# Kernel optimization log

Hardware: AMD Instinct MI355X
Metric: run time of the kernel (lower is better)

## Reference

```python
import jax, jax.numpy as jnp
import numpy as np

B, D, G, L = 8, 128, 2048, 24
GF = G // 2 + 1  # rfft bins
EPS = 1e-5


def setup_inputs() -> dict:
    key = jax.random.key(0)
    ks = jax.random.split(key, 6)
    x = jax.random.normal(ks[0], (B, D, G), dtype=jnp.float32)
    Phi_f = jax.random.normal(ks[1], (L, GF), dtype=jnp.float32) * 0.1
    Theta = jax.random.normal(ks[2], (L, D, D), dtype=jnp.float32) * (1.0 / np.sqrt(D))
    ln_gamma = jnp.ones((D,), dtype=jnp.float32)
    ln_beta = jnp.zeros((D,), dtype=jnp.float32)
    fc1_w = jax.random.normal(ks[3], (2 * D, D), dtype=jnp.float32) * (1.0 / np.sqrt(D))
    fc1_b = jnp.zeros((2 * D,), dtype=jnp.float32)
    fc2_w = jax.random.normal(ks[4], (D, 2 * D), dtype=jnp.float32) * (1.0 / np.sqrt(2 * D))
    fc2_b = jnp.zeros((D,), dtype=jnp.float32)
    return {
        'x': x, 'Phi_f': Phi_f, 'Theta': Theta,
        'ln_gamma': ln_gamma, 'ln_beta': ln_beta,
        'fc1_w': fc1_w, 'fc1_b': fc1_b, 'fc2_w': fc2_w, 'fc2_b': fc2_b,
    }


def reference(x, Phi_f, Theta, ln_gamma, ln_beta, fc1_w, fc1_b, fc2_w, fc2_b):
    # x: (B, D, G). LayerNorm over the lifting (channel) dim D.
    mean = jnp.mean(x, axis=1, keepdims=True)
    var = jnp.var(x, axis=1, keepdims=True)
    z = (x - mean) * jax.lax.rsqrt(var + EPS)
    z = z * ln_gamma[None, :, None] + ln_beta[None, :, None]

    # Spectral convolution with each Hilbert filter.
    Xf = jnp.fft.rfft(z, axis=-1)                       # (B, D, GF) complex
    Uf = Xf[:, :, None, :] * jnp.conj(Phi_f)[None, None]  # (B, D, L, GF)
    U = jnp.fft.irfft(Uf, n=G, axis=-1)                 # (B, D, L, G)

    # Per-filter channel mixing then reduction over filters:
    # einsum('bdln,lhd->bhln') followed by sum over l, fused:
    S = jnp.einsum('bdlg,lhd->bhg', U, Theta)           # (B, D, G)

    # Pointwise MLP (Conv1d kernel_size=1 == channel matmul).
    H = jnp.einsum('hd,bdg->bhg', fc1_w, S) + fc1_b[None, :, None]
    H = jax.nn.gelu(H, approximate=False)
    out = jnp.einsum('dh,bhg->bdg', fc2_w, H) + fc2_b[None, :, None]
    return x + out
```

## Files before the change

### kernel.cpp

```cpp
#include <hip/hip_runtime.h>
#include <math.h>


#define B_   8
#define D_   128
#define G_   2048
#define L_   24
#define GF_  1025
#define BD_  1024
#define DD_  16384
#define GQ_  512
#define CF4_ 514
#define MF4_ 576
#define NF4_ 4096

#define PA_CV0 256
#define PA_TT0 322
#define PA_WF0 578
#define PA_WI0 1154
#define PA_END 1666

#define G1_NB  576
#define G1_END 4800

typedef __attribute__((ext_vector_type(8))) short  short8v;
typedef __attribute__((ext_vector_type(4))) float  float4v;

union FU { float f; unsigned int u; };
union V8 { short8v v; ushort u[8]; };
union V4 { uint2 p; ushort u[4]; };

static __device__ __forceinline__ float bf2f(ushort h) {
    FU v; v.u = ((unsigned int)h) << 16; return v.f;
}
static __device__ __forceinline__ ushort f2bf(float f) {
    FU v; v.f = f;
    unsigned int r = v.u + 0x7fffu + ((v.u >> 16) & 1u);
    return (ushort)(r >> 16);
}
static __device__ __forceinline__ void async16(const void* g, void* l) {
    __builtin_amdgcn_global_load_lds(
        (const __attribute__((address_space(1))) void*)g,
        (__attribute__((address_space(3))) void*)l, 16, 0, 0);
}
static __device__ __forceinline__ int is_f32(const unsigned int* graw) {
    return graw[0] == 0x3F800000u;
}

__global__ __launch_bounds__(256) void k_pre(
        const void* __restrict__ x_raw,  const void* __restrict__ th_raw,
        const unsigned int* __restrict__ graw, const void* __restrict__ be_raw,
        const void* __restrict__ w1_raw, const void* __restrict__ b1_raw,
        const void* __restrict__ w2_raw, const void* __restrict__ b2_raw,
        ushort* __restrict__ z,  ushort* __restrict__ wf,
        ushort* __restrict__ wi, ushort* __restrict__ thT,
        ushort* __restrict__ w1c, ushort* __restrict__ b1c,
        ushort* __restrict__ w2c, ushort* __restrict__ b2c) {
    __shared__ ushort T[L_][72];
    __shared__ float red[2][256];
    __shared__ float mi[2][64];
    int bid = blockIdx.x, tid = threadIdx.x;

    if (bid < PA_CV0) {
        int fl = is_f32(graw);
        int b  = bid >> 5;
        int g0 = (bid & 31) * 64;
        int gi = tid & 63, dq = tid >> 6;
        int g  = g0 + gi;
        int d0 = dq * 32;
        float vals[32];
        float s = 0.f, ss = 0.f;
        if (fl) {
            const float* xp = (const float*)x_raw + (size_t)(b * D_ + d0) * G_ + g;
            #pragma unroll 8
            for (int d = 0; d < 32; ++d) {
                float v = xp[(size_t)d * G_];
                vals[d] = v; s += v; ss += v * v;
            }
        } else {
            const ushort* xp = (const ushort*)x_raw + (size_t)(b * D_ + d0) * G_ + g;
            #pragma unroll 8
            for (int d = 0; d < 32; ++d) {
                float v = bf2f(xp[(size_t)d * G_]);
                vals[d] = v; s += v; ss += v * v;
            }
        }
        red[0][tid] = s; red[1][tid] = ss;
        __syncthreads();
        if (tid < 64) {
            float S  = red[0][tid] + red[0][tid + 64] + red[0][tid + 128] +
                       red[0][tid + 192];
            float SS = red[1][tid] + red[1][tid + 64] + red[1][tid + 128] +
                       red[1][tid + 192];
            float mean = S * (1.f / D_);
            float var  = SS * (1.f / D_) - mean * mean;
            mi[0][tid] = mean;
            mi[1][tid] = rsqrtf(var + 1e-5f);
        }
        __syncthreads();
        float mean = mi[0][gi], inv = mi[1][gi];
        ushort* zp = z + (size_t)(g & 3) * (BD_ * GQ_) +
                     (size_t)(b * D_ + d0) * GQ_ + (g >> 2);
        if (fl) {
            const float* gp = (const float*)graw + d0;
            const float* bp = (const float*)be_raw + d0;
            #pragma unroll 8
            for (int d = 0; d < 32; ++d) {
                float o = (vals[d] - mean) * inv * gp[d] + bp[d];
                zp[(size_t)d * GQ_] = f2bf(o);
            }
        } else {
            const ushort* gp = (const ushort*)graw + d0;
            const ushort* bp = (const ushort*)be_raw + d0;
            #pragma unroll 8
            for (int d = 0; d < 32; ++d) {
                float o = (vals[d] - mean) * inv * bf2f(gp[d]) + bf2f(bp[d]);
                zp[(size_t)d * GQ_] = f2bf(o);
            }
        }
    } else if (bid < PA_TT0) {
        int fl = is_f32(graw);
        int lb = bid - PA_CV0;
        const void* src; ushort* dst; int n, rel;
        if (lb < 32)       { src = w1_raw; dst = w1c; n = 32768; rel = lb; }
        else if (lb == 32) { src = b1_raw; dst = b1c; n = 256;   rel = 0; }
        else if (lb < 65)  { src = w2_raw; dst = w2c; n = 32768; rel = lb - 33; }
        else               { src = b2_raw; dst = b2c; n = 128;   rel = 0; }
        int i0 = rel * 1024 + tid * 4;
        if (fl) {
            const float* s = (const float*)src;
            #pragma unroll
            for (int j = 0; j < 4; ++j) {
                int k = i0 + j;
                if (k < n) dst[k] = f2bf(s[k]);
            }
        } else {
            const ushort* s = (const ushort*)src;
            #pragma unroll
            for (int j = 0; j < 4; ++j) {
                int k = i0 + j;
                if (k < n) dst[k] = s[k];
            }
        }
    } else if (bid < PA_WF0) {
        int fl = is_f32(graw);
        int hd0 = (bid - PA_TT0) * 64;
        if (tid < 192) {
            int l = tid >> 3, c8 = tid & 7;
            V8 o;
            if (fl) {
                const float* tp = (const float*)th_raw + (size_t)l * DD_ +
                                  hd0 + c8 * 8;
                float4v a0 = *(const float4v*)tp;
                float4v a1 = *(const float4v*)(tp + 4);
                #pragma unroll
                for (int j = 0; j < 4; ++j) {
                    o.u[j] = f2bf(a0[j]); o.u[4 + j] = f2bf(a1[j]);
                }
            } else {
                o.v = *(const short8v*)((const ushort*)th_raw +
                                        (size_t)l * DD_ + hd0 + c8 * 8);
            }
            *(short8v*)&T[l][c8 * 8] = o.v;
        }
        __syncthreads();
        int hdl = tid & 63, part = tid >> 6;
        V8 o;
        #pragma unroll
        for (int j = 0; j < 8; ++j) {
            int l = part * 8 + j;
            o.u[j] = (l < L_) ? T[l][hdl] : (ushort)0;
        }
        *(short8v*)(thT + (size_t)(hd0 + hdl) * 32 + part * 8) = o.v;
    } else if (bid < PA_WI0) {
        int c = bid - PA_WF0;
        if (tid < 128) {
            int g0 = tid * 4;
            V4 v;
            if (c >= CF4_) {
                #pragma unroll
                for (int j = 0; j < 4; ++j) v.u[j] = 0;
            } else {
                int f = c >> 1, im = c & 1;
                #pragma unroll
                for (int j = 0; j < 4; ++j) {
                    int g = g0 + j;
                    int r = (f * g) & (GQ_ - 1);
                    float th = (float)r * 1.2271846303085130e-2f;
                    v.u[j] = f2bf(im ? -__sinf(th) : __cosf(th));
                }
            }
            *(uint2*)(wf + (size_t)c * GQ_ + g0) = v.p;
        }
    } else {
        int g = bid - PA_WI0;
        for (int ch = tid; ch < MF4_ / 8; ch += 256) {
            int c0 = ch * 8;
            V8 v;
            #pragma unroll
            for (int j = 0; j < 8; ++j) {
                int c = c0 + j;
                if (c >= CF4_) { v.u[j] = 0; continue; }
                int f = c >> 1, im = c & 1;
                float a = (f == 0 || f == GQ_ / 2) ? 4.8828125e-4f
                                                   : 9.765625e-4f;
                int r = (f * g) & (GQ_ - 1);
                float th = (float)r * 1.2271846303085130e-2f;
                v.u[j] = f2bf(im ? -a * __sinf(th) : a * __cosf(th));
            }
            *(short8v*)(wi + (size_t)g * MF4_ + c0) = v.v;
        }
    }
}

__global__ __launch_bounds__(256, 4) void k_g1(
        const ushort* __restrict__ wf, const ushort* __restrict__ z,
        ushort* __restrict__ zft,
        const void* __restrict__ phi_raw, const unsigned int* __restrict__ graw,
        const ushort* __restrict__ thT, ushort* __restrict__ M) {
    __shared__ ushort As[2][64 * 64];
    __shared__ ushort Bs[2][64 * 64];
    __shared__ ushort Aph[16][40];
    int bid = blockIdx.x, tid = threadIdx.x;
    int w = tid >> 6, lane = tid & 63;
    int lr = lane & 15, q = lane >> 4;

    if (bid < G1_NB) {
        int m0 = (bid >> 6) * 64;
        int n0 = (bid & 63) * 64;
        int wm = (w & 1) * 32, wn = (w >> 1) * 32;
        int rl = lane >> 3, c8 = (lane & 7) ^ rl;
        int t0 = w * 2, t1 = w * 2 + 1;
        const ushort* gA0 = wf + (size_t)(m0 + t0 * 8 + rl) * GQ_ + c8 * 8;
        const ushort* gA1 = wf + (size_t)(m0 + t1 * 8 + rl) * GQ_ + c8 * 8;
        const ushort* gB0 = z  + (size_t)(n0 + t0 * 8 + rl) * GQ_ + c8 * 8;
        const ushort* gB1 = z  + (size_t)(n0 + t1 * 8 + rl) * GQ_ + c8 * 8;

        float4v acc00 = {0.f,0.f,0.f,0.f}, acc01 = {0.f,0.f,0.f,0.f};
        float4v acc10 = {0.f,0.f,0.f,0.f}, acc11 = {0.f,0.f,0.f,0.f};

        async16(gA0, &As[0][t0 * 512]);
        async16(gA1, &As[0][t1 * 512]);
        async16(gB0, &Bs[0][t0 * 512]);
        async16(gB1, &Bs[0][t1 * 512]);
        __syncthreads();

        int buf = 0;
        for (int k0 = 0; k0 < GQ_; k0 += 64) {
            if (k0 + 64 < GQ_) {
                int nb = buf ^ 1;
                async16(gA0 + k0 + 64, &As[nb][t0 * 512]);
                async16(gA1 + k0 + 64, &As[nb][t1 * 512]);
                async16(gB0 + k0 + 64, &Bs[nb][t0 * 512]);
                async16(gB1 + k0 + 64, &Bs[nb][t1 * 512]);
            }
            const ushort* Ab = &As[buf][0];
            const ushort* Bb = &Bs[buf][0];
            #pragma unroll
            for (int s = 0; s < 2; ++s) {
                int cs = s * 4 + q;
                int ra0 = wm + lr, ra1 = wm + 16 + lr;
                int rb0 = wn + lr, rb1 = wn + 16 + lr;
                short8v a0 = *(const short8v*)(Ab + ra0 * 64 + ((cs ^ (ra0 & 7)) << 3));
                short8v a1 = *(const short8v*)(Ab + ra1 * 64 + ((cs ^ (ra1 & 7)) << 3));
                short8v b0 = *(const short8v*)(Bb + rb0 * 64 + ((cs ^ (rb0 & 7)) << 3));
                short8v b1 = *(const short8v*)(Bb + rb1 * 64 + ((cs ^ (rb1 & 7)) << 3));
                acc00 = __builtin_amdgcn_mfma_f32_16x16x32_bf16(a0, b0, acc00, 0, 0, 0);
                acc01 = __builtin_amdgcn_mfma_f32_16x16x32_bf16(a0, b1, acc01, 0, 0, 0);
                acc10 = __builtin_amdgcn_mfma_f32_16x16x32_bf16(a1, b0, acc10, 0, 0, 0);
                acc11 = __builtin_amdgcn_mfma_f32_16x16x32_bf16(a1, b1, acc11, 0, 0, 0);
            }
            __syncthreads();
            buf ^= 1;
        }

        float4v accs[2][2] = { { acc00, acc01 }, { acc10, acc11 } };
        #pragma unroll
        for (int i = 0; i < 2; ++i)
            #pragma unroll
            for (int j = 0; j < 2; ++j) {
                int col = n0 + wn + j * 16 + lr;
                int row = m0 + wm + i * 16 + q * 4;
                #pragma unroll
                for (int r = 0; r < 4; ++r)
                    zft[(size_t)(row + r) * NF4_ + col] = f2bf(accs[i][j][r]);
            }
    } else {
        int bb  = bid - G1_NB;
        int f0  = (bb >> 6) * 16;
        int hd0 = (bb & 63) * 256;
        int isf = is_f32(graw);
        #pragma unroll
        for (int rep = 0; rep < 2; ++rep) {
            int idx = rep * 256 + tid;
            int fl = idx >> 5, l = idx & 31;
            int f = f0 + fl;
            ushort v = 0;
            if (l < L_ && f < GF_)
                v = isf ? f2bf(((const float*)phi_raw)[(size_t)l * GF_ + f])
                        : ((const ushort*)phi_raw)[(size_t)l * GF_ + f];
            Aph[fl][l] = v;
        }
        __syncthreads();
        short8v a = *(const short8v*)&Aph[lr][q * 8];
        #pragma unroll
        for (int t = 0; t < 4; ++t) {
            int n = hd0 + (w * 4 + t) * 16 + lr;
            short8v b = *(const short8v*)(thT + (size_t)n * 32 + q * 8);
            float4v c = {0.f, 0.f, 0.f, 0.f};
            c = __builtin_amdgcn_mfma_f32_16x16x32_bf16(a, b, c, 0, 0, 0);
            #pragma unroll
            for (int r = 0; r < 4; ++r) {
                int f = f0 + q * 4 + r;
                if (f < GF_) M[(size_t)f * DD_ + n] = f2bf(c[r]);
            }
        }
    }
}

__global__ __launch_bounds__(256, 2) void k_mix3(const ushort* __restrict__ zft,
                                                 const ushort* __restrict__ M,
                                                 ushort* __restrict__ sft) {
    int bx  = blockIdx.x;
    int fp  = bx >> 1;
    int hh  = bx & 1;
    int tid = threadIdx.x;
    int w = tid >> 6, lane = tid & 63;
    int lr = lane & 15, q = lane >> 4;
    int cc = lr >> 3, bb = lr & 7;
    int ntg = hh * 4 + w;

    float a1 = (float)fp * 3.0679615757712823e-3f;
    float C1 = cosf(a1),        S1 = sinf(a1);
    float C2 = cosf(2.f * a1),  S2 = sinf(2.f * a1);
    float C3 = cosf(3.f * a1),  S3 = sinf(3.f * a1);

    float P01 = cc ? -S1 :  C1,  Q01 = cc ?  C1 :  S1;
    float P02 = cc ? -S2 :  C2,  Q02 = cc ?  C2 :  S2;
    float P03 = cc ? -S3 :  C3,  Q03 = cc ?  C3 :  S3;
    float P11 = cc ? -C1 :  S1,  Q11 = cc ? -S1 : -C1;
    float P12 = cc ? -S2 : -C2,  Q12 = cc ?  C2 : -S2;
    float P13 = cc ?  C3 : -S3,  Q13 = cc ?  S3 :  C3;
    float P21 = cc ? -C1 : -S1,  Q21 = cc ? -S1 :  C1;
    float P22 = cc ?  S2 : -C2,  Q22 = cc ? -C2 : -S2;
    float P23 = cc ?  C3 :  S3,  Q23 = cc ?  S3 : -C3;
    float P31 = cc ? -S1 : -C1,  Q31 = cc ?  C1 : -S1;
    float P32 = cc ?  S2 :  C2,  Q32 = cc ? -C2 :  S2;
    float P33 = cc ? -S3 : -C3,  Q33 = cc ?  C3 : -S3;

    const ushort* r0 = zft + (size_t)(2 * fp) * NF4_;
    const ushort* r1 = r0 + NF4_;
    int colb = bb * 128 + q * 8;

    short8v aZ[4][4];
    #pragma unroll
    for (int s = 0; s < 4; ++s) {
        int col = colb + s * 32;
        V8 R0, I0, R1, I1, R2, I2, R3, I3;
        R0.v = *(const short8v*)(r0 + col);
        I0.v = *(const short8v*)(r1 + col);
        R1.v = *(const short8v*)(r0 + 1024 + col);
        I1.v = *(const short8v*)(r1 + 1024 + col);
        R2.v = *(const short8v*)(r0 + 2048 + col);
        I2.v = *(const short8v*)(r1 + 2048 + col);
        R3.v = *(const short8v*)(r0 + 3072 + col);
        I3.v = *(const short8v*)(r1 + 3072 + col);
        V8 t0, t1, t2, t3;
        #pragma unroll
        for (int e = 0; e < 8; ++e) {
            float x0 = bf2f(R0.u[e]), y0 = bf2f(I0.u[e]);
            float x1 = bf2f(R1.u[e]), y1 = bf2f(I1.u[e]);
            float x2 = bf2f(R2.u[e]), y2 = bf2f(I2.u[e]);
            float x3 = bf2f(R3.u[e]), y3 = bf2f(I3.u[e]);
            float e0p = cc ?  y0 : x0;
            float e0m = cc ? -y0 : x0;
            float z0 = e0p, z1 = e0m, z2 = e0p, z3 = e0m;
            z0 = fmaf(P01, x1, z0); z0 = fmaf(Q01, y1, z0);
            z0 = fmaf(P02, x2, z0); z0 = fmaf(Q02, y2, z0);
            z0 = fmaf(P03, x3, z0); z0 = fmaf(Q03, y3, z0);
            z1 = fmaf(P11, x1, z1); z1 = fmaf(Q11, y1, z1);
            z1 = fmaf(P12, x2, z1); z1 = fmaf(Q12, y2, z1);
            z1 = fmaf(P13, x3, z1); z1 = fmaf(Q13, y3, z1);
            z2 = fmaf(P21, x1, z2); z2 = fmaf(Q21, y1, z2);
            z2 = fmaf(P22, x2, z2); z2 = fmaf(Q22, y2, z2);
            z2 = fmaf(P23, x3, z2); z2 = fmaf(Q23, y3, z2);
            z3 = fmaf(P31, x1, z3); z3 = fmaf(Q31, y1, z3);
            z3 = fmaf(P32, x2, z3); z3 = fmaf(Q32, y2, z3);
            z3 = fmaf(P33, x3, z3); z3 = fmaf(Q33, y3, z3);
            t0.u[e] = f2bf(z0); t1.u[e] = f2bf(z1);
            t2.u[e] = f2bf(z2); t3.u[e] = f2bf(z3);
        }
        aZ[0][s] = t0.v; aZ[1][s] = t1.v; aZ[2][s] = t2.v; aZ[3][s] = t3.v;
    }

    int fk0 = fp, fk1 = 512 - fp, fk2 = 512 + fp, fk3 = 1024 - fp;
    const ushort* Mp[4] = { M + (size_t)fk0 * DD_, M + (size_t)fk1 * DD_,
                            M + (size_t)fk2 * DD_, M + (size_t)fk3 * DD_ };
    float4v acc[4];
    #pragma unroll
    for (int k = 0; k < 4; ++k) {
        float4v c = {0.f, 0.f, 0.f, 0.f};
        #pragma unroll
        for (int s = 0; s < 4; ++s) {
            short8v bfr = *(const short8v*)(Mp[k] + (size_t)(ntg * 16 + lr) * D_ +
                                            s * 32 + q * 8);
            c = __builtin_amdgcn_mfma_f32_16x16x32_bf16(aZ[k][s], bfr, c, 0, 0, 0);
        }
        acc[k] = c;
    }

    #pragma unroll
    for (int e = 0; e < 4; ++e) {
        int p   = q * 4 + e;
        int c2i = p >> 3, cb = p & 7;
        float sg = c2i ? -1.f : 1.f;
        float u0 = acc[0][e], u1 = acc[1][e], u2 = acc[2][e], u3 = acc[3][e];
        float p1 = __shfl_xor(u1, 32);
        float p2 = __shfl_xor(u2, 32);
        float U0 = u0 + u2 + sg * (u1 + u3);
        float U1 = u0 - sg * p2 - sg * u3 - p1;
        float U2 = u0 - u2 + sg * (u3 - u1);
        float U3 = u0 + sg * p2 - sg * u3 + p1;
        float U1p = __shfl_xor(U1, 32);
        float U2p = __shfl_xor(U2, 32);
        float U3p = __shfl_xor(U3, 32);
        float T1 = fmaf(-sg * S1, U1p, C1 * U1);
        float T2 = fmaf(-sg * S2, U2p, C2 * U2);
        float T3 = fmaf(-sg * S3, U3p, C3 * U3);
        size_t base = (size_t)(2 * fp + c2i) * NF4_ + cb * 128 + ntg * 16 + lr;
        sft[base]          = f2bf(U0);
        sft[base + 1024]   = f2bf(T1);
        sft[base + 2048]   = f2bf(T2);
        sft[base + 3072]   = f2bf(T3);
    }
}

__global__ __launch_bounds__(256, 4) void k_gemm64t(const ushort* __restrict__ A,
                                                    const ushort* __restrict__ Bm,
                                                    ushort* __restrict__ C,
                                                    int K, int lda, int ldb,
                                                    int ldc, int kv) {
    __shared__ ushort As[2][64 * 64];
    __shared__ ushort Bs[2][64 * 64];
    int tid = threadIdx.x;
    int m0 = blockIdx.x * 64, n0 = blockIdx.y * 64;
    int w = tid >> 6, lane = tid & 63;
    int lr = lane & 15, q = lane >> 4;
    int wm = (w & 1) * 32, wn = (w >> 1) * 32;

    int rl = lane >> 3, c8 = (lane & 7) ^ rl;
    int t0 = w * 2, t1 = w * 2 + 1;
    const ushort* gA0 = A + (size_t)(m0 + t0 * 8 + rl) * lda + c8 * 8;
    const ushort* gA1 = A + (size_t)(m0 + t1 * 8 + rl) * lda + c8 * 8;

    int br = tid >> 2;
    int bc = tid & 3;

    float4v acc00 = {0.f,0.f,0.f,0.f}, acc01 = {0.f,0.f,0.f,0.f};
    float4v acc10 = {0.f,0.f,0.f,0.f}, acc11 = {0.f,0.f,0.f,0.f};

    async16(gA0, &As[0][t0 * 512]);
    async16(gA1, &As[0][t1 * 512]);
    {
        V8 u0, u1;
        if (br < kv) {
            const ushort* gb = Bm + (size_t)br * ldb + n0 + bc * 16;
            u0.v = *(const short8v*)gb;
            u1.v = *(const short8v*)(gb + 8);
        } else {
            #pragma unroll
            for (int j = 0; j < 8; ++j) { u0.u[j] = 0; u1.u[j] = 0; }
        }
        #pragma unroll
        for (int j = 0; j < 8; ++j) {
            int n = bc * 16 + j;
            Bs[0][n * 64 + ((((br >> 3) ^ (n & 7)) << 3) | (br & 7))] = u0.u[j];
        }
        #pragma unroll
        for (int j = 0; j < 8; ++j) {
            int n = bc * 16 + 8 + j;
            Bs[0][n * 64 + ((((br >> 3) ^ (n & 7)) << 3) | (br & 7))] = u1.u[j];
        }
    }
    __syncthreads();

    int buf = 0;
    for (int k0 = 0; k0 < K; k0 += 64) {
        V8 u0, u1;
        bool more = (k0 + 64 < K);
        if (more) {
            int nb = buf ^ 1;
            async16(gA0 + k0 + 64, &As[nb][t0 * 512]);
            async16(gA1 + k0 + 64, &As[nb][t1 * 512]);
            int kr = k0 + 64 + br;
            if (kr < kv) {
                const ushort* gb = Bm + (size_t)kr * ldb + n0 + bc * 16;
                u0.v = *(const short8v*)gb;
                u1.v = *(const short8v*)(gb + 8);
            } else {
                #pragma unroll
                for (int j = 0; j < 8; ++j) { u0.u[j] = 0; u1.u[j] = 0; }
            }
        }
        const ushort* Ab = &As[buf][0];
        const ushort* Bb = &Bs[buf][0];
        #pragma unroll
        for (int s = 0; s < 2; ++s) {
            int cs = s * 4 + q;
            int ra0 = wm + lr, ra1 = wm + 16 + lr;
            int rb0 = wn + lr, rb1 = wn + 16 + lr;
            short8v a0 = *(const short8v*)(Ab + ra0 * 64 + ((cs ^ (ra0 & 7)) << 3));
            short8v a1 = *(const short8v*)(Ab + ra1 * 64 + ((cs ^ (ra1 & 7)) << 3));
            short8v b0 = *(const short8v*)(Bb + rb0 * 64 + ((cs ^ (rb0 & 7)) << 3));
            short8v b1 = *(const short8v*)(Bb + rb1 * 64 + ((cs ^ (rb1 & 7)) << 3));
            acc00 = __builtin_amdgcn_mfma_f32_16x16x32_bf16(a0, b0, acc00, 0, 0, 0);
            acc01 = __builtin_amdgcn_mfma_f32_16x16x32_bf16(a0, b1, acc01, 0, 0, 0);
            acc10 = __builtin_amdgcn_mfma_f32_16x16x32_bf16(a1, b0, acc10, 0, 0, 0);
            acc11 = __builtin_amdgcn_mfma_f32_16x16x32_bf16(a1, b1, acc11, 0, 0, 0);
        }
        __syncthreads();
        if (more) {
            int nb = buf ^ 1;
            #pragma unroll
            for (int j = 0; j < 8; ++j) {
                int n = bc * 16 + j;
                Bs[nb][n * 64 + ((((br >> 3) ^ (n & 7)) << 3) | (br & 7))] = u0.u[j];
            }
            #pragma unroll
            for (int j = 0; j < 8; ++j) {
                int n = bc * 16 + 8 + j;
                Bs[nb][n * 64 + ((((br >> 3) ^ (n & 7)) << 3) | (br & 7))] = u1.u[j];
            }
        }
        __syncthreads();
        buf ^= 1;
    }

    float4v accs[2][2] = { { acc00, acc01 }, { acc10, acc11 } };
    #pragma unroll
    for (int i = 0; i < 2; ++i)
        #pragma unroll
        for (int j = 0; j < 2; ++j) {
            int col = n0 + wn + j * 16 + lr;
            int row = m0 + wm + i * 16 + q * 4;
            #pragma unroll
            for (int r = 0; r < 4; ++r)
                C[(size_t)(row + r) * ldc + col] = f2bf(accs[i][j][r]);
        }
}

#define MLPG 32
__global__ __launch_bounds__(256, 2) void k_mlp3(const ushort* __restrict__ ST,
                                                 const void* __restrict__ x0,
                                                 const ushort* __restrict__ w1,
                                                 const ushort* __restrict__ b1,
                                                 const ushort* __restrict__ w2,
                                                 const ushort* __restrict__ b2,
                                                 const unsigned int* __restrict__ graw,
                                                 void* __restrict__ outv) {
    __shared__ ushort Sb[MLPG][136];
    __shared__ ushort Hb[MLPG][264];
    __shared__ float  Ob[128][36];
    int g0 = blockIdx.x * MLPG, b = blockIdx.y;
    int tid = threadIdx.x;
    {
        int col = tid >> 3, seg = tid & 7;
        int g = g0 + col;
        const ushort* sp = ST + (size_t)(g >> 2) * NF4_ + (g & 3) * BD_ +
                           b * D_ + seg * 16;
        short8v s0 = *(const short8v*)(sp);
        short8v s1 = *(const short8v*)(sp + 8);
        *(short8v*)&Sb[col][seg * 16]     = s0;
        *(short8v*)&Sb[col][seg * 16 + 8] = s1;
    }
    __syncthreads();
    int w = tid >> 6, lane = tid & 63;
    int lr = lane & 15, q = lane >> 4;
    int nt = w & 1, mh = w >> 1;

    {
        float4v acc[8];
        #pragma unroll
        for (int i = 0; i < 8; ++i) { float4v zz = {0.f,0.f,0.f,0.f}; acc[i] = zz; }
        #pragma unroll
        for (int ks = 0; ks < 4; ++ks) {
            short8v bf = *(const short8v*)&Sb[nt * 16 + lr][ks * 32 + q * 8];
            #pragma unroll
            for (int i = 0; i < 8; ++i) {
                int mt = mh * 8 + i;
                short8v af = *(const short8v*)(w1 + (size_t)(mt * 16 + lr) * D_ +
                                               ks * 32 + q * 8);
                acc[i] = __builtin_amdgcn_mfma_f32_16x16x32_bf16(af, bf, acc[i], 0, 0, 0);
            }
        }
        #pragma unroll
        for (int i = 0; i < 8; ++i) {
            int h0 = (mh * 8 + i) * 16 + q * 4;
            V4 hv;
            #pragma unroll
            for (int r = 0; r < 4; ++r) {
                float v = acc[i][r] + bf2f(b1[h0 + r]);
                v = 0.5f * v * (1.f + erff(v * 0.70710678118f));
                hv.u[r] = f2bf(v);
            }
            *(uint2*)&Hb[nt * 16 + lr][h0] = hv.p;
        }
    }
    __syncthreads();
    {
        float4v acc2[4];
        #pragma unroll
        for (int j = 0; j < 4; ++j) { float4v zz = {0.f,0.f,0.f,0.f}; acc2[j] = zz; }
        #pragma unroll
        for (int ks = 0; ks < 8; ++ks) {
            short8v bf = *(const short8v*)&Hb[nt * 16 + lr][ks * 32 + q * 8];
            #pragma unroll
            for (int j = 0; j < 4; ++j) {
                int mt2 = mh * 4 + j;
                short8v af = *(const short8v*)(w2 + (size_t)(mt2 * 16 + lr) * (2 * D_) +
                                               ks * 32 + q * 8);
                acc2[j] = __builtin_amdgcn_mfma_f32_16x16x32_bf16(af, bf, acc2[j], 0, 0, 0);
            }
        }
        int col = nt * 16 + lr;
        #pragma unroll
        for (int j = 0; j < 4; ++j) {
            int d0 = (mh * 4 + j) * 16 + q * 4;
            #pragma unroll
            for (int r = 0; r < 4; ++r)
                Ob[d0 + r][col] = acc2[j][r] + bf2f(b2[d0 + r]);
        }
    }
    __syncthreads();
    {
        int fl = is_f32(graw);
        if (fl) {
            #pragma unroll
            for (int p = 0; p < 4; ++p) {
                int idx = p * 256 + tid;
                int d = idx >> 3, c4 = (idx & 7) * 4;
                float4v o = *(const float4v*)&Ob[d][c4];
                size_t gidx = ((size_t)(b * D_ + d)) * G_ + g0 + c4;
                float4v xv = *(const float4v*)((const float*)x0 + gidx);
                float4v ov;
                #pragma unroll
                for (int k = 0; k < 4; ++k) ov[k] = o[k] + xv[k];
                *(float4v*)((float*)outv + gidx) = ov;
            }
        } else {
            #pragma unroll
            for (int p = 0; p < 4; ++p) {
                int idx = p * 256 + tid;
                int d = idx >> 3, c4 = (idx & 7) * 4;
                float4v o = *(const float4v*)&Ob[d][c4];
                size_t gidx = ((size_t)(b * D_ + d)) * G_ + g0 + c4;
                V4 xv; xv.p = *(const uint2*)((const ushort*)x0 + gidx);
                V4 ov;
                #pragma unroll
                for (int k = 0; k < 4; ++k) ov.u[k] = f2bf(o[k] + bf2f(xv.u[k]));
                *(uint2*)((ushort*)outv + gidx) = ov.p;
            }
        }
    }
}

extern "C" void kernel_launch(void* const* d_in, const int* in_sizes, int n_in,
                              void* d_out, int out_size, void* d_ws, size_t ws_size,
                              hipStream_t stream) {
    char* base = (char*)d_ws;
    ushort* z    = (ushort*)(base);
    ushort* wf   = (ushort*)(base + 4194304);
    ushort* sft  = (ushort*)(base);
    ushort* zft  = (ushort*)(base + 13107200);
    ushort* st   = (ushort*)(base + 13107200);
    ushort* w1c  = (ushort*)(base + 27050048);
    ushort* b1c  = (ushort*)(base + 27115584);
    ushort* w2c  = (ushort*)(base + 27116096);
    ushort* b2c  = (ushort*)(base + 27181632);
    ushort* Mm   = (ushort*)(base + 27182592);
    ushort* wi   = (ushort*)(base + 60769792);
    ushort* thT  = (ushort*)(base + 69420544);

    const unsigned int* graw = (const unsigned int*)d_in[3];

    k_pre    <<<dim3(PA_END), 256, 0, stream>>>(
        d_in[0], d_in[2], graw, d_in[4], d_in[5], d_in[6], d_in[7], d_in[8],
        z, wf, wi, thT, w1c, b1c, w2c, b2c);
    k_g1     <<<dim3(G1_END), 256, 0, stream>>>(wf, z, zft, d_in[1], graw,
                                                thT, Mm);
    k_mix3   <<<dim3(514), 256, 0, stream>>>(zft, Mm, sft);
    k_gemm64t<<<dim3(GQ_ / 64, NF4_ / 64), 256, 0, stream>>>(
        wi, sft, st, MF4_, MF4_, NF4_, NF4_, CF4_);
    k_mlp3   <<<dim3(G_ / MLPG, B_), 256, 0, stream>>>(st, d_in[0], w1c, b1c,
                                                       w2c, b2c, graw, d_out);
}
```

Measured before the change: 157.5 us.

## Pack real DFT coefficients into 512 rows, dropping zero imaginary rows

The forward and inverse DFT twiddle matrices now use a packed layout with 512 coefficient rows instead of 576 padded rows (514 used). The always-zero imaginary parts at DC and Nyquist are dropped and the Nyquist real part is stored in the last slot. The mixing kernel remaps its row indices to match and zeroes the imaginary inputs at DC and Nyquist, so the GEMM K dimension and the first-stage GEMM row blocks shrink. The mixing kernel's launch bounds also rise to 3 blocks per SM. This removes padded work, but the mixing kernel now has aliased row handling to keep correct.

```diff
diff --git a/kernel.cpp b/kernel.cpp
--- a/kernel.cpp
+++ b/kernel.cpp
@@ -10,18 +10,17 @@
 #define BD_  1024
 #define DD_  16384
 #define GQ_  512
-#define CF4_ 514
-#define MF4_ 576
+#define MC_  512
 #define NF4_ 4096
 
 #define PA_CV0 256
 #define PA_TT0 322
 #define PA_WF0 578
-#define PA_WI0 1154
-#define PA_END 1666
-
-#define G1_NB  576
-#define G1_END 4800
+#define PA_WI0 1090
+#define PA_END 1602
+
+#define G1_NB  512
+#define G1_END 4736
 
 typedef __attribute__((ext_vector_type(8))) short  short8v;
 typedef __attribute__((ext_vector_type(4))) float  float4v;
@@ -45,6 +44,10 @@
 }
 static __device__ __forceinline__ int is_f32(const unsigned int* graw) {
     return graw[0] == 0x3F800000u;
+}
+static __device__ __forceinline__ void crow_inv(int c, int& f, int& im) {
+    if (c == 0) { f = 0; im = 0; }
+    else        { f = (c + 1) >> 1; im = (c + 1) & 1; }
 }
 
 __global__ __launch_bounds__(256) void k_pre(
@@ -175,40 +178,34 @@
     } else if (bid < PA_WI0) {
         int c = bid - PA_WF0;
         if (tid < 128) {
+            int f, im; crow_inv(c, f, im);
             int g0 = tid * 4;
             V4 v;
-            if (c >= CF4_) {
-                #pragma unroll
-                for (int j = 0; j < 4; ++j) v.u[j] = 0;
-            } else {
-                int f = c >> 1, im = c & 1;
-                #pragma unroll
-                for (int j = 0; j < 4; ++j) {
-                    int g = g0 + j;
-                    int r = (f * g) & (GQ_ - 1);
-                    float th = (float)r * 1.2271846303085130e-2f;
-                    v.u[j] = f2bf(im ? -__sinf(th) : __cosf(th));
-                }
+            #pragma unroll
+            for (int j = 0; j < 4; ++j) {
+                int g = g0 + j;
+                int r = (f * g) & (GQ_ - 1);
+                float th = (float)r * 1.2271846303085130e-2f;
+                v.u[j] = f2bf(im ? -__sinf(th) : __cosf(th));
             }
             *(uint2*)(wf + (size_t)c * GQ_ + g0) = v.p;
         }
     } else {
         int g = bid - PA_WI0;
-        for (int ch = tid; ch < MF4_ / 8; ch += 256) {
+        for (int ch = tid; ch < MC_ / 8; ch += 256) {
             int c0 = ch * 8;
             V8 v;
             #pragma unroll
             for (int j = 0; j < 8; ++j) {
                 int c = c0 + j;
-                if (c >= CF4_) { v.u[j] = 0; continue; }
-                int f = c >> 1, im = c & 1;
+                int f, im; crow_inv(c, f, im);
                 float a = (f == 0 || f == GQ_ / 2) ? 4.8828125e-4f
                                                    : 9.765625e-4f;
                 int r = (f * g) & (GQ_ - 1);
                 float th = (float)r * 1.2271846303085130e-2f;
                 v.u[j] = f2bf(im ? -a * __sinf(th) : a * __cosf(th));
             }
-            *(short8v*)(wi + (size_t)g * MF4_ + c0) = v.v;
+            *(short8v*)(wi + (size_t)g * MC_ + c0) = v.v;
         }
     }
 }
@@ -318,7 +315,7 @@
     }
 }
 
-__global__ __launch_bounds__(256, 2) void k_mix3(const ushort* __restrict__ zft,
+__global__ __launch_bounds__(256, 3) void k_mix3(const ushort* __restrict__ zft,
                                                  const ushort* __restrict__ M,
                                                  ushort* __restrict__ sft) {
     int bx  = blockIdx.x;
@@ -329,6 +326,10 @@
     int lr = lane & 15, q = lane >> 4;
     int cc = lr >> 3, bb = lr & 7;
     int ntg = hh * 4 + w;
+
+    int rowRe  = (fp == 0) ? 0 : (fp == 256 ? 511 : 2 * fp - 1);
+    int rowIm  = (fp == 0 || fp == 256) ? rowRe : 2 * fp;
+    bool has_im = (fp != 0) && (fp != 256);
 
     float a1 = (float)fp * 3.0679615757712823e-3f;
     float C1 = cosf(a1),        S1 = sinf(a1);
@@ -348,8 +349,8 @@
     float P32 = cc ?  S2 :  C2,  Q32 = cc ? -C2 :  S2;
     float P33 = cc ? -S3 : -C3,  Q33 = cc ?  C3 : -S3;
 
-    const ushort* r0 = zft + (size_t)(2 * fp) * NF4_;
-    const ushort* r1 = r0 + NF4_;
+    const ushort* r0 = zft + (size_t)rowRe * NF4_;
+    const ushort* r1 = zft + (size_t)rowIm * NF4_;
     int colb = bb * 128 + q * 8;
 
     short8v aZ[4][4];
@@ -365,6 +366,12 @@
         I2.v = *(const short8v*)(r1 + 2048 + col);
         R3.v = *(const short8v*)(r0 + 3072 + col);
         I3.v = *(const short8v*)(r1 + 3072 + col);
+        if (!has_im) {
+            #pragma unroll
+            for (int e = 0; e < 8; ++e) {
+                I0.u[e] = 0; I1.u[e] = 0; I2.u[e] = 0; I3.u[e] = 0;
+            }
+        }
         V8 t0, t1, t2, t3;
         #pragma unroll
         for (int e = 0; e < 8; ++e) {
@@ -427,11 +434,14 @@
         float T1 = fmaf(-sg * S1, U1p, C1 * U1);
         float T2 = fmaf(-sg * S2, U2p, C2 * U2);
         float T3 = fmaf(-sg * S3, U3p, C3 * U3);
-        size_t base = (size_t)(2 * fp + c2i) * NF4_ + cb * 128 + ntg * 16 + lr;
-        sft[base]          = f2bf(U0);
-        sft[base + 1024]   = f2bf(T1);
-        sft[base + 2048]   = f2bf(T2);
-        sft[base + 3072]   = f2bf(T3);
+        int orow = c2i ? rowIm : rowRe;
+        if (has_im || c2i == 0) {
+            size_t base = (size_t)orow * NF4_ + cb * 128 + ntg * 16 + lr;
+            sft[base]          = f2bf(U0);
+            sft[base + 1024]   = f2bf(T1);
+            sft[base + 2048]   = f2bf(T2);
+            sft[base + 3072]   = f2bf(T3);
+        }
     }
 }
 
@@ -690,7 +700,7 @@
                                                 thT, Mm);
     k_mix3   <<<dim3(514), 256, 0, stream>>>(zft, Mm, sft);
     k_gemm64t<<<dim3(GQ_ / 64, NF4_ / 64), 256, 0, stream>>>(
-        wi, sft, st, MF4_, MF4_, NF4_, NF4_, CF4_);
+        wi, sft, st, MC_, MC_, NF4_, NF4_, MC_);
     k_mlp3   <<<dim3(G_ / MLPG, B_), 256, 0, stream>>>(st, d_in[0], w1c, b1c,
                                                        w2c, b2c, graw, d_out);
 }
```

Result: slower. 163.7 us (+3.9%).
